# Kernel tuning notes

Hardware: AMD Instinct MI355X
Metric: run time of the kernel (lower is better)

Reference implementation:

```python
import jax, jax.numpy as jnp
import numpy as np

N, E, F, H, L, G = 100000, 1600000, 32, 128, 4, 64


def gru_cell(m, h, w_ih, b_ih, w_hh, b_hh):
    # torch.nn.GRUCell math; gate order: r, z, n
    gi = m @ w_ih.T + b_ih          # [N, 3H]
    gh = h @ w_hh.T + b_hh          # [N, 3H]
    i_r, i_z, i_n = jnp.split(gi, 3, axis=-1)
    h_r, h_z, h_n = jnp.split(gh, 3, axis=-1)
    r = jax.nn.sigmoid(i_r + h_r)
    z = jax.nn.sigmoid(i_z + h_z)
    n = jnp.tanh(i_n + r * h_n)
    return (1.0 - z) * n + z * h


def setup_inputs() -> dict:
    key = jax.random.key(0)
    ks = jax.random.split(key, 12)
    s = 0.05
    return {
        "x": jax.random.normal(ks[0], (N, F), jnp.float32),
        "edge_index": jax.random.randint(ks[1], (2, E), 0, N, jnp.int64),
        "batch": jnp.sort(jax.random.randint(ks[2], (N,), 0, G, jnp.int64)),
        "num_graphs": G,
        "W0": jax.random.normal(ks[3], (H, F), jnp.float32) * s,
        "conv_w": jax.random.normal(ks[4], (L, H, H), jnp.float32) * s,
        "w_ih": jax.random.normal(ks[5], (3 * H, H), jnp.float32) * s,
        "b_ih": jax.random.normal(ks[6], (3 * H,), jnp.float32) * s,
        "w_hh": jax.random.normal(ks[7], (3 * H, H), jnp.float32) * s,
        "b_hh": jax.random.normal(ks[8], (3 * H,), jnp.float32) * s,
        "lin1_w": jax.random.normal(ks[9], (1, H), jnp.float32) * s,
        "lin1_b": jax.random.normal(ks[10], (1,), jnp.float32) * s,
    }


def reference(x, edge_index, batch, num_graphs, W0, conv_w, w_ih, b_ih, w_hh, b_hh, lin1_w, lin1_b):
    n_nodes = x.shape[0]
    # lin0 (no bias) + sigmoid embedding
    x_embed = jax.nn.sigmoid(x @ W0.T)                     # [N, H]

    src, dst = edge_index[0], edge_index[1]
    h = x_embed
    # GatedGraphConv: per layer, transform -> scatter-add over edges -> GRU update
    for l in range(conv_w.shape[0]):
        m = h @ conv_w[l]                                   # [N, H]
        agg = jax.ops.segment_sum(m[src], dst, num_segments=n_nodes)  # [N, H]
        h = gru_cell(agg, h, w_ih, b_ih, w_hh, b_hh)

    h = jax.nn.relu(h)
    out = h @ lin1_w.T + lin1_b                             # [N, 1]
    uncorrected = out

    # per-graph mean subtraction (scatter_mean + gather), same math as the loop
    sums = jax.ops.segment_sum(out, batch, num_segments=num_graphs)   # [G, 1]
    counts = jax.ops.segment_sum(jnp.ones((n_nodes, 1), out.dtype), batch, num_segments=num_graphs)
    mean_all = sums / jnp.maximum(counts, 1.0)
    corrected = out - mean_all[batch]

    return corrected.squeeze(1), x_embed, uncorrected.squeeze(1)
```

## Files before the change

### kernel.cpp

```cpp
#include <hip/hip_runtime.h>
#include <hip/hip_bf16.h>

#define HDIM 128
#define FDIM 32
#define GGR  64
#define SCAN_CHUNK 2048
#define FILL_CHUNK 1024
#define FILL_WIN 16

typedef __attribute__((ext_vector_type(8))) short bf16x8;
typedef __attribute__((ext_vector_type(4))) float f32x4;

__device__ __forceinline__ float fsig(float x) {
  return __builtin_amdgcn_rcpf(1.f + __expf(-x));
}
__device__ __forceinline__ float ftanh(float x) {
  return 1.f - 2.f * __builtin_amdgcn_rcpf(1.f + __expf(2.f * x));
}

__device__ __forceinline__ bf16x8 pack_bf16x8(float4 a, float4 b) {
  union { bf16x8 v; __hip_bfloat162 h[4]; } u;
  u.h[0] = __float22bfloat162_rn(make_float2(a.x, a.y));
  u.h[1] = __float22bfloat162_rn(make_float2(a.z, a.w));
  u.h[2] = __float22bfloat162_rn(make_float2(b.x, b.y));
  u.h[3] = __float22bfloat162_rn(make_float2(b.z, b.w));
  return u.v;
}

__device__ __forceinline__ int ablk(int kb, int m) {
  return (kb << 6) + (m & 56) + ((m ^ kb) & 7);
}

__device__ __forceinline__ void stage64(const unsigned short* __restrict__ g,
                                        short* __restrict__ s, int n0, int N, int t) {
#pragma unroll
  for (int r = 0; r < 2; ++r) {
    int idx = r * 512 + t;
    int m = idx >> 4, c8 = idx & 15;
    int gn = n0 + m;
    uint4 v = make_uint4(0u, 0u, 0u, 0u);
    if (gn < N) v = *(const uint4*)(g + (size_t)gn * HDIM + c8 * 8);
    *(uint4*)(s + ablk(c8, m) * 8) = v;
  }
}


__global__ __launch_bounds__(256) void k_embed_hist(const float* __restrict__ x,
                                                    const unsigned short* __restrict__ W0b,
                                                    unsigned short* __restrict__ hb,
                                                    float* __restrict__ xemb,
                                                    const unsigned short* __restrict__ convT0,
                                                    unsigned short* __restrict__ m_out,
                                                    int N,
                                                    const int* __restrict__ dst,
                                                    int* __restrict__ deg,
                                                    unsigned short* __restrict__ rank,
                                                    long long E, int histBlocks, int q8) {
  __shared__ short sE[16 * 64 * 8];
  if ((int)blockIdx.x < histBlocks) {
    long long e = (long long)blockIdx.x * 256 + threadIdx.x;
    if (e < E) {
      int old = atomicAdd(&deg[dst[e]], 1);
      rank[e] = (unsigned short)old;
    }
    return;
  }
  int p = blockIdx.x - histBlocks;
  int T = (p & 7) * q8 + (p >> 3);
  int n0 = T * 64;
  if (n0 >= N) return;
  int t = threadIdx.x;
  int w = t >> 6, l = t & 63;
  int lm = l & 15, lq = l >> 4;
  int j0 = w * 32;
  bf16x8 b0 = *(const bf16x8*)(W0b + (size_t)(j0 + lm) * FDIM + lq * 8);
  bf16x8 b1 = *(const bf16x8*)(W0b + (size_t)(j0 + 16 + lm) * FDIM + lq * 8);
  f32x4 acc0[4], acc1[4];
#pragma unroll
  for (int i = 0; i < 4; ++i) { acc0[i] = (f32x4){0.f,0.f,0.f,0.f}; acc1[i] = (f32x4){0.f,0.f,0.f,0.f}; }
#pragma unroll
  for (int tt = 0; tt < 4; ++tt) {
    int rg = n0 + tt * 16 + lm;
    bf16x8 a = (bf16x8){0,0,0,0,0,0,0,0};
    if (rg < N) {
      const float4* xr = (const float4*)x + (size_t)rg * 8 + lq * 2;
      a = pack_bf16x8(xr[0], xr[1]);
    }
    acc0[tt] = __builtin_amdgcn_mfma_f32_16x16x32_bf16(a, b0, acc0[tt], 0, 0, 0);
    acc1[tt] = __builtin_amdgcn_mfma_f32_16x16x32_bf16(a, b1, acc1[tt], 0, 0, 0);
  }
#pragma unroll
  for (int g = 0; g < 2; ++g) {
    int j = j0 + g * 16 + lm;
#pragma unroll
    for (int tt = 0; tt < 4; ++tt)
#pragma unroll
      for (int r = 0; r < 4; ++r) {
        int m = tt * 16 + lq * 4 + r;
        int node = n0 + m;
        float v = g ? acc1[tt][r] : acc0[tt][r];
        float e = fsig(v);
        __hip_bfloat16 eb = __float2bfloat16(e);
        ((__hip_bfloat16*)sE)[ablk(j >> 3, m) * 8 + (j & 7)] = eb;
        if (node < N) {
          size_t off = (size_t)node * HDIM + j;
          xemb[off] = e;
          ((__hip_bfloat16*)hb)[off] = eb;
        }
      }
  }
  __syncthreads();
#pragma unroll
  for (int g = 0; g < 2; ++g) {
    int jg = j0 + g * 16;
    f32x4 macc[4];
#pragma unroll
    for (int i = 0; i < 4; ++i) macc[i] = (f32x4){0.f,0.f,0.f,0.f};
#pragma unroll
    for (int ks = 0; ks < 4; ++ks) {
      bf16x8 b = *(const bf16x8*)(convT0 + (size_t)(jg + lm) * HDIM + ks * 32 + lq * 8);
      int kb = ks * 4 + lq;
#pragma unroll
      for (int tt = 0; tt < 4; ++tt) {
        bf16x8 a = *(const bf16x8*)(sE + ablk(kb, tt * 16 + lm) * 8);
        macc[tt] = __builtin_amdgcn_mfma_f32_16x16x32_bf16(a, b, macc[tt], 0, 0, 0);
      }
    }
    int j = jg + lm;
#pragma unroll
    for (int tt = 0; tt < 4; ++tt)
#pragma unroll
      for (int r = 0; r < 4; ++r) {
        int node = n0 + tt * 16 + lq * 4 + r;
        if (node < N)
          ((__hip_bfloat16*)m_out)[(size_t)node * HDIM + j] = __float2bfloat16(macc[tt][r]);
      }
  }
}

__global__ __launch_bounds__(256) void k_prep_w(const float* __restrict__ w_ih,
                                                const float* __restrict__ w_hh,
                                                const float* __restrict__ conv_w,
                                                const float* __restrict__ W0,
                                                unsigned short* __restrict__ wIb,
                                                unsigned short* __restrict__ wHb,
                                                unsigned short* __restrict__ convTb,
                                                unsigned short* __restrict__ W0b,
                                                int L) {
  int i = blockIdx.x * 256 + threadIdx.x;
  if (i < HDIM * FDIM) ((__hip_bfloat16*)W0b)[i] = __float2bfloat16(W0[i]);
  if (i < 384 * HDIM) {
    ((__hip_bfloat16*)wIb)[i] = __float2bfloat16(w_ih[i]);
    ((__hip_bfloat16*)wHb)[i] = __float2bfloat16(w_hh[i]);
  }
  int total = L * HDIM * HDIM;
  if (i < total) {
    int l = i >> 14, rem = i & 16383, j = rem >> 7, k = rem & 127;
    ((__hip_bfloat16*)convTb)[i] = __float2bfloat16(conv_w[(l << 14) + (k << 7) + j]);
  }
}

__global__ __launch_bounds__(256) void k_block_sum(const int* __restrict__ deg,
                                                   int* __restrict__ bsum, int N) {
  int base = blockIdx.x * SCAN_CHUNK + threadIdx.x * 8;
  int s = 0;
#pragma unroll
  for (int u = 0; u < 8; ++u) { int i = base + u; if (i < N) s += deg[i]; }
#pragma unroll
  for (int o = 32; o; o >>= 1) s += __shfl_down(s, o, 64);
  __shared__ int wsum[4];
  if ((threadIdx.x & 63) == 0) wsum[threadIdx.x >> 6] = s;
  __syncthreads();
  if (threadIdx.x == 0) bsum[blockIdx.x] = wsum[0] + wsum[1] + wsum[2] + wsum[3];
}

__global__ void k_scan_bsums(int* __restrict__ bsum, int nb) {
  if (blockIdx.x == 0 && threadIdx.x == 0) {
    int run = 0;
    for (int i = 0; i < nb; ++i) { int v = bsum[i]; bsum[i] = run; run += v; }
  }
}

__global__ __launch_bounds__(256) void k_scan_chunks(const int* __restrict__ deg,
                                                     const int* __restrict__ bsum,
                                                     int* __restrict__ rowstart,
                                                     int N, int Etot) {
  __shared__ int ts[256];
  int base = blockIdx.x * SCAN_CHUNK + threadIdx.x * 8;
  int loc[8]; int s = 0;
#pragma unroll
  for (int u = 0; u < 8; ++u) {
    int i = base + u; loc[u] = s;
    s += (i < N) ? deg[i] : 0;
  }
  ts[threadIdx.x] = s;
  __syncthreads();
  for (int o = 1; o < 256; o <<= 1) {
    int v = (threadIdx.x >= o) ? ts[threadIdx.x - o] : 0;
    __syncthreads();
    ts[threadIdx.x] += v;
    __syncthreads();
  }
  int texcl = (threadIdx.x ? ts[threadIdx.x - 1] : 0) + bsum[blockIdx.x];
#pragma unroll
  for (int u = 0; u < 8; ++u) {
    int i = base + u;
    if (i < N) rowstart[i] = texcl + loc[u];
  }
  if (blockIdx.x == 0 && threadIdx.x == 0) rowstart[N] = Etot;
}

__global__ __launch_bounds__(256) void k_csr_fill_win(const int* __restrict__ src,
                                                      const int* __restrict__ dst,
                                                      const unsigned short* __restrict__ rank,
                                                      const int* __restrict__ rowstart,
                                                      int* __restrict__ csr,
                                                      long long E, int N) {
  __shared__ int sd[FILL_CHUNK];
  __shared__ int ss[FILL_CHUNK];
  __shared__ unsigned short sr[FILL_CHUNK];
  long long base = (long long)blockIdx.x * FILL_CHUNK;
  int cnt = (int)((E - base < FILL_CHUNK) ? (E - base) : FILL_CHUNK);
  for (int i = threadIdx.x; i < cnt; i += 256) {
    sd[i] = dst[base + i];
    ss[i] = src[base + i];
    sr[i] = rank[base + i];
  }
  __syncthreads();
  int nw = (N + FILL_WIN - 1) / FILL_WIN;
#pragma unroll 1
  for (int w = 0; w < FILL_WIN; ++w) {
    int lo = w * nw, hi = lo + nw;
    for (int i = threadIdx.x; i < cnt; i += 256) {
      int d = sd[i];
      if (d >= lo && d < hi)
        csr[rowstart[d] + sr[i]] = ss[i];
    }
    __syncthreads();
  }
}

__global__ __launch_bounds__(256) void k_gather(const int* __restrict__ csr,
                                                const int* __restrict__ rowstart,
                                                const unsigned short* __restrict__ m,
                                                unsigned short* __restrict__ agg, int N, int q8) {
  int p = blockIdx.x;
  int G = (p & 7) * q8 * 16 + (p >> 3);
  int wv = threadIdx.x >> 6, l = threadIdx.x & 63;
  int n = G * 4 + wv;
  if (n >= N) return;
  int eq = l >> 3;
  int jb = l & 7;
  int beg = rowstart[n], end = rowstart[n + 1];
  float acc[16];
#pragma unroll
  for (int i = 0; i < 16; ++i) acc[i] = 0.f;
  for (int e0 = beg; e0 < end; e0 += 8) {
    int e = e0 + eq;
    uint4 v0 = make_uint4(0u, 0u, 0u, 0u);
    uint4 v1 = make_uint4(0u, 0u, 0u, 0u);
    if (e < end) {
      int s = csr[e];
      const uint4* row = (const uint4*)(m + (size_t)s * HDIM + jb * 16);
      v0 = row[0];
      v1 = row[1];
    }
    acc[0]  += __uint_as_float(v0.x << 16);
    acc[1]  += __uint_as_float(v0.x & 0xffff0000u);
    acc[2]  += __uint_as_float(v0.y << 16);
    acc[3]  += __uint_as_float(v0.y & 0xffff0000u);
    acc[4]  += __uint_as_float(v0.z << 16);
    acc[5]  += __uint_as_float(v0.z & 0xffff0000u);
    acc[6]  += __uint_as_float(v0.w << 16);
    acc[7]  += __uint_as_float(v0.w & 0xffff0000u);
    acc[8]  += __uint_as_float(v1.x << 16);
    acc[9]  += __uint_as_float(v1.x & 0xffff0000u);
    acc[10] += __uint_as_float(v1.y << 16);
    acc[11] += __uint_as_float(v1.y & 0xffff0000u);
    acc[12] += __uint_as_float(v1.z << 16);
    acc[13] += __uint_as_float(v1.z & 0xffff0000u);
    acc[14] += __uint_as_float(v1.w << 16);
    acc[15] += __uint_as_float(v1.w & 0xffff0000u);
  }
#pragma unroll
  for (int i = 0; i < 16; ++i) {
    acc[i] += __shfl_xor(acc[i], 8, 64);
    acc[i] += __shfl_xor(acc[i], 16, 64);
    acc[i] += __shfl_xor(acc[i], 32, 64);
  }
  if (eq == 0) {
    union { uint4 v[2]; __hip_bfloat162 h[8]; } o;
#pragma unroll
    for (int i = 0; i < 8; ++i)
      o.h[i] = __float22bfloat162_rn(make_float2(acc[2 * i], acc[2 * i + 1]));
    uint4* dstp = (uint4*)(agg + (size_t)n * HDIM + jb * 16);
    dstp[0] = o.v[0];
    dstp[1] = o.v[1];
  }
}

__global__ __launch_bounds__(512, 4) void k_gru_mfma(const unsigned short* __restrict__ aggb,
                                                  const unsigned short* __restrict__ hb,
                                                  const unsigned short* __restrict__ wI,
                                                  const unsigned short* __restrict__ wH,
                                                  const float* __restrict__ b_ih,
                                                  const float* __restrict__ b_hh,
                                                  unsigned short* __restrict__ hnewb,
                                                  const unsigned short* __restrict__ wT,
                                                  unsigned short* __restrict__ m_out,
                                                  int N, int q8) {
  __shared__ short sAg[16 * 64 * 8];
  __shared__ short sH[16 * 64 * 8];
  int p = blockIdx.x;
  int T = (p & 7) * q8 + (p >> 3);
  int n0 = T * 64;
  if (n0 >= N) return;
  int t = threadIdx.x;
  stage64(aggb, sAg, n0, N, t);
  stage64(hb, sH, n0, N, t);
  int w = t >> 6, l = t & 63;
  int j0 = w * 16;
  int lm = l & 15, lq = l >> 4;
  int j = j0 + lm;
  float bir = b_ih[j], biz = b_ih[j + 128], bin = b_ih[j + 256];
  float bhr = b_hh[j], bhz = b_hh[j + 128], bhn = b_hh[j + 256];
  __syncthreads();
  f32x4 aR[4], aZ[4], aNi[4], aNh[4];
#pragma unroll
  for (int i = 0; i < 4; ++i) {
    aR[i] = (f32x4){0.f,0.f,0.f,0.f}; aZ[i] = (f32x4){0.f,0.f,0.f,0.f};
    aNi[i] = (f32x4){0.f,0.f,0.f,0.f}; aNh[i] = (f32x4){0.f,0.f,0.f,0.f};
  }
#pragma unroll
  for (int ks = 0; ks < 4; ++ks) {
    size_t rI = (size_t)(j0 + lm) * HDIM + ks * 32 + lq * 8;
    bf16x8 bIr = *(const bf16x8*)(wI + rI);
    bf16x8 bIz = *(const bf16x8*)(wI + rI + 128 * HDIM);
    bf16x8 bIn = *(const bf16x8*)(wI + rI + 256 * HDIM);
    bf16x8 bHr = *(const bf16x8*)(wH + rI);
    bf16x8 bHz = *(const bf16x8*)(wH + rI + 128 * HDIM);
    bf16x8 bHn = *(const bf16x8*)(wH + rI + 256 * HDIM);
    int kb = ks * 4 + lq;
#pragma unroll
    for (int tt = 0; tt < 4; ++tt) {
      bf16x8 a = *(const bf16x8*)(sAg + ablk(kb, tt * 16 + lm) * 8);
      bf16x8 h = *(const bf16x8*)(sH + ablk(kb, tt * 16 + lm) * 8);
      aR[tt] = __builtin_amdgcn_mfma_f32_16x16x32_bf16(a, bIr, aR[tt], 0, 0, 0);
      aR[tt] = __builtin_amdgcn_mfma_f32_16x16x32_bf16(h, bHr, aR[tt], 0, 0, 0);
      aZ[tt] = __builtin_amdgcn_mfma_f32_16x16x32_bf16(a, bIz, aZ[tt], 0, 0, 0);
      aZ[tt] = __builtin_amdgcn_mfma_f32_16x16x32_bf16(h, bHz, aZ[tt], 0, 0, 0);
      aNi[tt] = __builtin_amdgcn_mfma_f32_16x16x32_bf16(a, bIn, aNi[tt], 0, 0, 0);
      aNh[tt] = __builtin_amdgcn_mfma_f32_16x16x32_bf16(h, bHn, aNh[tt], 0, 0, 0);
    }
  }
  __syncthreads();
#pragma unroll
  for (int tt = 0; tt < 4; ++tt)
#pragma unroll
    for (int r = 0; r < 4; ++r) {
      int m = tt * 16 + lq * 4 + r;
      int node = n0 + m;
      float hp = __bfloat162float(((const __hip_bfloat16*)sH)[ablk(j >> 3, m) * 8 + (j & 7)]);
      float rg = fsig(aR[tt][r] + bir + bhr);
      float zg = fsig(aZ[tt][r] + biz + bhz);
      float nv = aNi[tt][r] + bin + rg * (aNh[tt][r] + bhn);
      float th = ftanh(nv);
      float hn = (1.f - zg) * th + zg * hp;
      __hip_bfloat16 hnb = __float2bfloat16(hn);
      ((__hip_bfloat16*)sAg)[ablk(j >> 3, m) * 8 + (j & 7)] = hnb;
      if (node < N)
        ((__hip_bfloat16*)hnewb)[(size_t)node * HDIM + j] = hnb;
    }
  __syncthreads();
  f32x4 macc[4];
#pragma unroll
  for (int i = 0; i < 4; ++i) macc[i] = (f32x4){0.f,0.f,0.f,0.f};
#pragma unroll
  for (int ks = 0; ks < 4; ++ks) {
    bf16x8 b = *(const bf16x8*)(wT + (size_t)(j0 + lm) * HDIM + ks * 32 + lq * 8);
    int kb = ks * 4 + lq;
#pragma unroll
    for (int tt = 0; tt < 4; ++tt) {
      bf16x8 a = *(const bf16x8*)(sAg + ablk(kb, tt * 16 + lm) * 8);
      macc[tt] = __builtin_amdgcn_mfma_f32_16x16x32_bf16(a, b, macc[tt], 0, 0, 0);
    }
  }
#pragma unroll
  for (int tt = 0; tt < 4; ++tt)
#pragma unroll
    for (int r = 0; r < 4; ++r) {
      int node = n0 + tt * 16 + lq * 4 + r;
      if (node < N)
        ((__hip_bfloat16*)m_out)[(size_t)node * HDIM + j] = __float2bfloat16(macc[tt][r]);
    }
}

__global__ __launch_bounds__(512, 4) void k_gru_last(const unsigned short* __restrict__ aggb,
                                                  const unsigned short* __restrict__ hb,
                                                  const unsigned short* __restrict__ wI,
                                                  const unsigned short* __restrict__ wH,
                                                  const float* __restrict__ b_ih,
                                                  const float* __restrict__ b_hh,
                                                  const float* __restrict__ w1,
                                                  const float* __restrict__ b1,
                                                  float* __restrict__ out_raw,
                                                  float* __restrict__ out_unc,
                                                  int N, int q8) {
  __shared__ short sAg[16 * 64 * 8];
  __shared__ short sH[16 * 64 * 8];
  __shared__ float sOut[64];
  int p = blockIdx.x;
  int T = (p & 7) * q8 + (p >> 3);
  int n0 = T * 64;
  if (n0 >= N) return;
  int t = threadIdx.x;
  stage64(aggb, sAg, n0, N, t);
  stage64(hb, sH, n0, N, t);
  if (t < 64) sOut[t] = 0.f;
  int w = t >> 6, l = t & 63;
  int j0 = w * 16;
  int lm = l & 15, lq = l >> 4;
  int j = j0 + lm;
  float bir = b_ih[j], biz = b_ih[j + 128], bin = b_ih[j + 256];
  float bhr = b_hh[j], bhz = b_hh[j + 128], bhn = b_hh[j + 256];
  float w1j = w1[j];
  __syncthreads();
  f32x4 aR[4], aZ[4], aNi[4], aNh[4];
#pragma unroll
  for (int i = 0; i < 4; ++i) {
    aR[i] = (f32x4){0.f,0.f,0.f,0.f}; aZ[i] = (f32x4){0.f,0.f,0.f,0.f};
    aNi[i] = (f32x4){0.f,0.f,0.f,0.f}; aNh[i] = (f32x4){0.f,0.f,0.f,0.f};
  }
#pragma unroll
  for (int ks = 0; ks < 4; ++ks) {
    size_t rI = (size_t)(j0 + lm) * HDIM + ks * 32 + lq * 8;
    bf16x8 bIr = *(const bf16x8*)(wI + rI);
    bf16x8 bIz = *(const bf16x8*)(wI + rI + 128 * HDIM);
    bf16x8 bIn = *(const bf16x8*)(wI + rI + 256 * HDIM);
    bf16x8 bHr = *(const bf16x8*)(wH + rI);
    bf16x8 bHz = *(const bf16x8*)(wH + rI + 128 * HDIM);
    bf16x8 bHn = *(const bf16x8*)(wH + rI + 256 * HDIM);
    int kb = ks * 4 + lq;
#pragma unroll
    for (int tt = 0; tt < 4; ++tt) {
      bf16x8 a = *(const bf16x8*)(sAg + ablk(kb, tt * 16 + lm) * 8);
      bf16x8 h = *(const bf16x8*)(sH + ablk(kb, tt * 16 + lm) * 8);
      aR[tt] = __builtin_amdgcn_mfma_f32_16x16x32_bf16(a, bIr, aR[tt], 0, 0, 0);
      aR[tt] = __builtin_amdgcn_mfma_f32_16x16x32_bf16(h, bHr, aR[tt], 0, 0, 0);
      aZ[tt] = __builtin_amdgcn_mfma_f32_16x16x32_bf16(a, bIz, aZ[tt], 0, 0, 0);
      aZ[tt] = __builtin_amdgcn_mfma_f32_16x16x32_bf16(h, bHz, aZ[tt], 0, 0, 0);
      aNi[tt] = __builtin_amdgcn_mfma_f32_16x16x32_bf16(a, bIn, aNi[tt], 0, 0, 0);
      aNh[tt] = __builtin_amdgcn_mfma_f32_16x16x32_bf16(h, bHn, aNh[tt], 0, 0, 0);
    }
  }
  __syncthreads();
#pragma unroll
  for (int tt = 0; tt < 4; ++tt)
#pragma unroll
    for (int r = 0; r < 4; ++r) {
      int m = tt * 16 + lq * 4 + r;
      int node = n0 + m;
      float hp = __bfloat162float(((const __hip_bfloat16*)sH)[ablk(j >> 3, m) * 8 + (j & 7)]);
      float rg = fsig(aR[tt][r] + bir + bhr);
      float zg = fsig(aZ[tt][r] + biz + bhz);
      float nv = aNi[tt][r] + bin + rg * (aNh[tt][r] + bhn);
      float th = ftanh(nv);
      float hn = (1.f - zg) * th + zg * hp;
      float prt = (node < N) ? fmaxf(hn, 0.f) * w1j : 0.f;
      prt += __shfl_xor(prt, 1, 64);
      prt += __shfl_xor(prt, 2, 64);
      prt += __shfl_xor(prt, 4, 64);
      prt += __shfl_xor(prt, 8, 64);
      if (lm == 0) atomicAdd(&sOut[m], prt);
    }
  __syncthreads();
  if (t < 64) {
    int node = n0 + t;
    if (node < N) {
      float o = sOut[t] + b1[0];
      out_raw[node] = o;
      out_unc[node] = o;
    }
  }
}

__global__ __launch_bounds__(256) void k_graph_reduce(const float* __restrict__ out_raw,
                                                      const int* __restrict__ batch,
                                                      float* __restrict__ gsum,
                                                      float* __restrict__ gcnt,
                                                      int N) {
  __shared__ float ls[GGR], lc[GGR];
  int t = threadIdx.x;
  if (t < GGR) { ls[t] = 0.f; lc[t] = 0.f; }
  __syncthreads();
  for (int n = blockIdx.x * 256 + t; n < N; n += gridDim.x * 256) {
    int g = batch[n];
    atomicAdd(&ls[g], out_raw[n]);
    atomicAdd(&lc[g], 1.f);
  }
  __syncthreads();
  if (t < GGR) {
    unsafeAtomicAdd(&gsum[t], ls[t]);
    unsafeAtomicAdd(&gcnt[t], lc[t]);
  }
}

__global__ __launch_bounds__(256) void k_correct(const float* __restrict__ out_raw,
                                                 const int* __restrict__ batch,
                                                 const float* __restrict__ gsum,
                                                 const float* __restrict__ gcnt,
                                                 float* __restrict__ corrected, int N) {
  int n = blockIdx.x * 256 + threadIdx.x;
  if (n < N) {
    int g = batch[n];
    corrected[n] = out_raw[n] - gsum[g] / fmaxf(gcnt[g], 1.f);
  }
}

extern "C" void kernel_launch(void* const* d_in, const int* in_sizes, int n_in,
                              void* d_out, int out_size, void* d_ws, size_t ws_size,
                              hipStream_t stream) {
  const float* x      = (const float*)d_in[0];
  const int*   ei     = (const int*)d_in[1];
  const int*   batch  = (const int*)d_in[2];
  const float* W0     = (const float*)d_in[4];
  const float* conv_w = (const float*)d_in[5];
  const float* w_ih   = (const float*)d_in[6];
  const float* b_ih   = (const float*)d_in[7];
  const float* w_hh   = (const float*)d_in[8];
  const float* b_hh   = (const float*)d_in[9];
  const float* lin1_w = (const float*)d_in[10];
  const float* lin1_b = (const float*)d_in[11];

  int N = in_sizes[0] / FDIM;
  long long E = in_sizes[1] / 2;
  int L = in_sizes[5] / (HDIM * HDIM);

  const int* src = ei;
  const int* dstv = ei + E;

  float* out_corrected = (float*)d_out;
  float* out_xemb = out_corrected + N;
  float* out_unc  = out_xemb + (size_t)N * HDIM;

  char* p = (char*)d_ws;
  unsigned short* x0 = (unsigned short*)p; p += (size_t)N * HDIM * 2;
  unsigned short* x1 = (unsigned short*)p; p += (size_t)N * HDIM * 2;
  unsigned short* x2 = (unsigned short*)p; p += (size_t)N * HDIM * 2;
  float* out_raw = (float*)p;        p += (size_t)((N + 3) & ~3) * 4;
  float* gsum = (float*)p;           p += GGR * 4;
  float* gcnt = (float*)p;           p += GGR * 4;
  int* deg = (int*)p;                p += (size_t)((N + 3) & ~3) * 4;
  int* rowstart = (int*)p;           p += (size_t)(N + 4) * 4;
  int nb = (N + SCAN_CHUNK - 1) / SCAN_CHUNK;
  int* bsum = (int*)p;               p += (size_t)((nb + 63) & ~63) * 4;
  int* csr = (int*)p;                p += (size_t)E * 4;
  unsigned short* rankb = (unsigned short*)p;  p += (size_t)((E + 3) & ~3) * 2;
  unsigned short* wIb = (unsigned short*)p;    p += 384 * HDIM * 2;
  unsigned short* wHb = (unsigned short*)p;    p += 384 * HDIM * 2;
  unsigned short* convTb = (unsigned short*)p; p += (size_t)L * HDIM * HDIM * 2;
  unsigned short* W0b = (unsigned short*)p;

  int prep_total = (384 * HDIM > L * HDIM * HDIM) ? 384 * HDIM : L * HDIM * HDIM;
  k_prep_w<<<(prep_total + 255) / 256, 256, 0, stream>>>(w_ih, w_hh, conv_w, W0, wIb, wHb, convTb, W0b, L);

  hipMemsetAsync(deg, 0, (size_t)N * sizeof(int), stream);
  hipMemsetAsync(gsum, 0, 2 * GGR * sizeof(float), stream);

  int nblk = (N + 63) / 64;
  int TP = (nblk + 7) & ~7;
  int q8 = TP / 8;
  int histBlocks = (int)((E + 255) / 256);
  k_embed_hist<<<histBlocks + TP, 256, 0, stream>>>(x, W0b, x0, out_xemb, convTb, x1, N,
                                                    dstv, deg, rankb, E, histBlocks, q8);

  k_block_sum<<<nb, 256, 0, stream>>>(deg, bsum, N);
  k_scan_bsums<<<1, 64, 0, stream>>>(bsum, nb);
  k_scan_chunks<<<nb, 256, 0, stream>>>(deg, bsum, rowstart, N, (int)E);
  k_csr_fill_win<<<(int)((E + FILL_CHUNK - 1) / FILL_CHUNK), 256, 0, stream>>>(
      src, dstv, rankb, rowstart, csr, E, N);

  unsigned short* Hb = x0;
  unsigned short* Mb = x1;
  for (int l = 0; l < L; ++l) {
    k_gather<<<TP * 16, 256, 0, stream>>>(csr, rowstart, Mb, x2, N, q8);
    if (l + 1 < L) {
      const unsigned short* wTn = convTb + (size_t)(l + 1) * HDIM * HDIM;
      k_gru_mfma<<<TP, 512, 0, stream>>>(x2, Hb, wIb, wHb, b_ih, b_hh, Mb, wTn, Hb, N, q8);
      unsigned short* tmp = Hb; Hb = Mb; Mb = tmp;
    } else {
      k_gru_last<<<TP, 512, 0, stream>>>(x2, Hb, wIb, wHb, b_ih, b_hh,
                                         lin1_w, lin1_b, out_raw, out_unc, N, q8);
    }
  }

  k_graph_reduce<<<256, 256, 0, stream>>>(out_raw, batch, gsum, gcnt, N);
  k_correct<<<(N + 255) / 256, 256, 0, stream>>>(out_raw, batch, gsum, gcnt, out_corrected, N);
}
```

Before: 731.7 us.

## Gather raw hidden states then apply conv weight after aggregation

Uses linearity of the sum over edges: gather and sum h directly, then multiply the summed rows by conv_w[l] inside the GRU kernel, instead of computing m = h@W before the gather. This drops the m_out write from the embed and GRU kernels, along with the separate message buffer. The gather now reads h, and the GRU kernel does one extra 64x128x128 MFMA pass plus extra syncs at its start. Rounding changes because the bf16 sum of h is quantized before the matmul.

```diff
diff --git a/kernel.cpp b/kernel.cpp
--- a/kernel.cpp
+++ b/kernel.cpp
@@ -49,14 +49,11 @@
                                                     const unsigned short* __restrict__ W0b,
                                                     unsigned short* __restrict__ hb,
                                                     float* __restrict__ xemb,
-                                                    const unsigned short* __restrict__ convT0,
-                                                    unsigned short* __restrict__ m_out,
                                                     int N,
                                                     const int* __restrict__ dst,
                                                     int* __restrict__ deg,
                                                     unsigned short* __restrict__ rank,
                                                     long long E, int histBlocks, int q8) {
-  __shared__ short sE[16 * 64 * 8];
   if ((int)blockIdx.x < histBlocks) {
     long long e = (long long)blockIdx.x * 256 + threadIdx.x;
     if (e < E) {
@@ -96,44 +93,14 @@
     for (int tt = 0; tt < 4; ++tt)
 #pragma unroll
       for (int r = 0; r < 4; ++r) {
-        int m = tt * 16 + lq * 4 + r;
-        int node = n0 + m;
-        float v = g ? acc1[tt][r] : acc0[tt][r];
-        float e = fsig(v);
-        __hip_bfloat16 eb = __float2bfloat16(e);
-        ((__hip_bfloat16*)sE)[ablk(j >> 3, m) * 8 + (j & 7)] = eb;
+        int node = n0 + tt * 16 + lq * 4 + r;
         if (node < N) {
+          float v = g ? acc1[tt][r] : acc0[tt][r];
+          float e = fsig(v);
           size_t off = (size_t)node * HDIM + j;
           xemb[off] = e;
-          ((__hip_bfloat16*)hb)[off] = eb;
+          ((__hip_bfloat16*)hb)[off] = __float2bfloat16(e);
         }
-      }
-  }
-  __syncthreads();
-#pragma unroll
-  for (int g = 0; g < 2; ++g) {
-    int jg = j0 + g * 16;
-    f32x4 macc[4];
-#pragma unroll
-    for (int i = 0; i < 4; ++i) macc[i] = (f32x4){0.f,0.f,0.f,0.f};
-#pragma unroll
-    for (int ks = 0; ks < 4; ++ks) {
-      bf16x8 b = *(const bf16x8*)(convT0 + (size_t)(jg + lm) * HDIM + ks * 32 + lq * 8);
-      int kb = ks * 4 + lq;
-#pragma unroll
-      for (int tt = 0; tt < 4; ++tt) {
-        bf16x8 a = *(const bf16x8*)(sE + ablk(kb, tt * 16 + lm) * 8);
-        macc[tt] = __builtin_amdgcn_mfma_f32_16x16x32_bf16(a, b, macc[tt], 0, 0, 0);
-      }
-    }
-    int j = jg + lm;
-#pragma unroll
-    for (int tt = 0; tt < 4; ++tt)
-#pragma unroll
-      for (int r = 0; r < 4; ++r) {
-        int node = n0 + tt * 16 + lq * 4 + r;
-        if (node < N)
-          ((__hip_bfloat16*)m_out)[(size_t)node * HDIM + j] = __float2bfloat16(macc[tt][r]);
       }
   }
 }
@@ -299,15 +266,14 @@
   }
 }
 
-__global__ __launch_bounds__(512, 4) void k_gru_mfma(const unsigned short* __restrict__ aggb,
+__global__ __launch_bounds__(512, 4) void k_gru_mfma(const unsigned short* __restrict__ hsum,
                                                   const unsigned short* __restrict__ hb,
+                                                  const unsigned short* __restrict__ wT,
                                                   const unsigned short* __restrict__ wI,
                                                   const unsigned short* __restrict__ wH,
                                                   const float* __restrict__ b_ih,
                                                   const float* __restrict__ b_hh,
                                                   unsigned short* __restrict__ hnewb,
-                                                  const unsigned short* __restrict__ wT,
-                                                  unsigned short* __restrict__ m_out,
                                                   int N, int q8) {
   __shared__ short sAg[16 * 64 * 8];
   __shared__ short sH[16 * 64 * 8];
@@ -316,7 +282,7 @@
   int n0 = T * 64;
   if (n0 >= N) return;
   int t = threadIdx.x;
-  stage64(aggb, sAg, n0, N, t);
+  stage64(hsum, sAg, n0, N, t);
   stage64(hb, sH, n0, N, t);
   int w = t >> 6, l = t & 63;
   int j0 = w * 16;
@@ -324,6 +290,30 @@
   int j = j0 + lm;
   float bir = b_ih[j], biz = b_ih[j + 128], bin = b_ih[j + 256];
   float bhr = b_hh[j], bhz = b_hh[j + 128], bhn = b_hh[j + 256];
+  __syncthreads();
+  {
+    f32x4 macc[4];
+#pragma unroll
+    for (int i = 0; i < 4; ++i) macc[i] = (f32x4){0.f,0.f,0.f,0.f};
+#pragma unroll
+    for (int ks = 0; ks < 4; ++ks) {
+      bf16x8 b = *(const bf16x8*)(wT + (size_t)(j0 + lm) * HDIM + ks * 32 + lq * 8);
+      int kb = ks * 4 + lq;
+#pragma unroll
+      for (int tt = 0; tt < 4; ++tt) {
+        bf16x8 a = *(const bf16x8*)(sAg + ablk(kb, tt * 16 + lm) * 8);
+        macc[tt] = __builtin_amdgcn_mfma_f32_16x16x32_bf16(a, b, macc[tt], 0, 0, 0);
+      }
+    }
+    __syncthreads();
+#pragma unroll
+    for (int tt = 0; tt < 4; ++tt)
+#pragma unroll
+      for (int r = 0; r < 4; ++r) {
+        int m = tt * 16 + lq * 4 + r;
+        ((__hip_bfloat16*)sAg)[ablk(j >> 3, m) * 8 + (j & 7)] = __float2bfloat16(macc[tt][r]);
+      }
+  }
   __syncthreads();
   f32x4 aR[4], aZ[4], aNi[4], aNh[4];
 #pragma unroll
@@ -353,7 +343,6 @@
       aNh[tt] = __builtin_amdgcn_mfma_f32_16x16x32_bf16(h, bHn, aNh[tt], 0, 0, 0);
     }
   }
-  __syncthreads();
 #pragma unroll
   for (int tt = 0; tt < 4; ++tt)
 #pragma unroll
@@ -366,37 +355,14 @@
       float nv = aNi[tt][r] + bin + rg * (aNh[tt][r] + bhn);
       float th = ftanh(nv);
       float hn = (1.f - zg) * th + zg * hp;
-      __hip_bfloat16 hnb = __float2bfloat16(hn);
-      ((__hip_bfloat16*)sAg)[ablk(j >> 3, m) * 8 + (j & 7)] = hnb;
       if (node < N)
-        ((__hip_bfloat16*)hnewb)[(size_t)node * HDIM + j] = hnb;
-    }
-  __syncthreads();
-  f32x4 macc[4];
-#pragma unroll
-  for (int i = 0; i < 4; ++i) macc[i] = (f32x4){0.f,0.f,0.f,0.f};
-#pragma unroll
-  for (int ks = 0; ks < 4; ++ks) {
-    bf16x8 b = *(const bf16x8*)(wT + (size_t)(j0 + lm) * HDIM + ks * 32 + lq * 8);
-    int kb = ks * 4 + lq;
-#pragma unroll
-    for (int tt = 0; tt < 4; ++tt) {
-      bf16x8 a = *(const bf16x8*)(sAg + ablk(kb, tt * 16 + lm) * 8);
-      macc[tt] = __builtin_amdgcn_mfma_f32_16x16x32_bf16(a, b, macc[tt], 0, 0, 0);
-    }
-  }
-#pragma unroll
-  for (int tt = 0; tt < 4; ++tt)
-#pragma unroll
-    for (int r = 0; r < 4; ++r) {
-      int node = n0 + tt * 16 + lq * 4 + r;
-      if (node < N)
-        ((__hip_bfloat16*)m_out)[(size_t)node * HDIM + j] = __float2bfloat16(macc[tt][r]);
-    }
-}
-
-__global__ __launch_bounds__(512, 4) void k_gru_last(const unsigned short* __restrict__ aggb,
+        ((__hip_bfloat16*)hnewb)[(size_t)node * HDIM + j] = __float2bfloat16(hn);
+    }
+}
+
+__global__ __launch_bounds__(512, 4) void k_gru_last(const unsigned short* __restrict__ hsum,
                                                   const unsigned short* __restrict__ hb,
+                                                  const unsigned short* __restrict__ wT,
                                                   const unsigned short* __restrict__ wI,
                                                   const unsigned short* __restrict__ wH,
                                                   const float* __restrict__ b_ih,
@@ -414,7 +380,7 @@
   int n0 = T * 64;
   if (n0 >= N) return;
   int t = threadIdx.x;
-  stage64(aggb, sAg, n0, N, t);
+  stage64(hsum, sAg, n0, N, t);
   stage64(hb, sH, n0, N, t);
   if (t < 64) sOut[t] = 0.f;
   int w = t >> 6, l = t & 63;
@@ -424,6 +390,30 @@
   float bir = b_ih[j], biz = b_ih[j + 128], bin = b_ih[j + 256];
   float bhr = b_hh[j], bhz = b_hh[j + 128], bhn = b_hh[j + 256];
   float w1j = w1[j];
+  __syncthreads();
+  {
+    f32x4 macc[4];
+#pragma unroll
+    for (int i = 0; i < 4; ++i) macc[i] = (f32x4){0.f,0.f,0.f,0.f};
+#pragma unroll
+    for (int ks = 0; ks < 4; ++ks) {
+      bf16x8 b = *(const bf16x8*)(wT + (size_t)(j0 + lm) * HDIM + ks * 32 + lq * 8);
+      int kb = ks * 4 + lq;
+#pragma unroll
+      for (int tt = 0; tt < 4; ++tt) {
+        bf16x8 a = *(const bf16x8*)(sAg + ablk(kb, tt * 16 + lm) * 8);
+        macc[tt] = __builtin_amdgcn_mfma_f32_16x16x32_bf16(a, b, macc[tt], 0, 0, 0);
+      }
+    }
+    __syncthreads();
+#pragma unroll
+    for (int tt = 0; tt < 4; ++tt)
+#pragma unroll
+      for (int r = 0; r < 4; ++r) {
+        int m = tt * 16 + lq * 4 + r;
+        ((__hip_bfloat16*)sAg)[ablk(j >> 3, m) * 8 + (j & 7)] = __float2bfloat16(macc[tt][r]);
+      }
+  }
   __syncthreads();
   f32x4 aR[4], aZ[4], aNi[4], aNh[4];
 #pragma unroll
@@ -571,7 +561,7 @@
   int TP = (nblk + 7) & ~7;
   int q8 = TP / 8;
   int histBlocks = (int)((E + 255) / 256);
-  k_embed_hist<<<histBlocks + TP, 256, 0, stream>>>(x, W0b, x0, out_xemb, convTb, x1, N,
+  k_embed_hist<<<histBlocks + TP, 256, 0, stream>>>(x, W0b, x0, out_xemb, N,
                                                     dstv, deg, rankb, E, histBlocks, q8);
 
   k_block_sum<<<nb, 256, 0, stream>>>(deg, bsum, N);
@@ -581,15 +571,15 @@
       src, dstv, rankb, rowstart, csr, E, N);
 
   unsigned short* Hb = x0;
-  unsigned short* Mb = x1;
+  unsigned short* Fb = x1;
   for (int l = 0; l < L; ++l) {
-    k_gather<<<TP * 16, 256, 0, stream>>>(csr, rowstart, Mb, x2, N, q8);
+    k_gather<<<TP * 16, 256, 0, stream>>>(csr, rowstart, Hb, x2, N, q8);
+    const unsigned short* wTl = convTb + (size_t)l * HDIM * HDIM;
     if (l + 1 < L) {
-      const unsigned short* wTn = convTb + (size_t)(l + 1) * HDIM * HDIM;
-      k_gru_mfma<<<TP, 512, 0, stream>>>(x2, Hb, wIb, wHb, b_ih, b_hh, Mb, wTn, Hb, N, q8);
-      unsigned short* tmp = Hb; Hb = Mb; Mb = tmp;
+      k_gru_mfma<<<TP, 512, 0, stream>>>(x2, Hb, wTl, wIb, wHb, b_ih, b_hh, Fb, N, q8);
+      unsigned short* tmp = Hb; Hb = Fb; Fb = tmp;
     } else {
-      k_gru_last<<<TP, 512, 0, stream>>>(x2, Hb, wIb, wHb, b_ih, b_hh,
+      k_gru_last<<<TP, 512, 0, stream>>>(x2, Hb, wTl, wIb, wHb, b_ih, b_hh,
                                          lin1_w, lin1_b, out_raw, out_unc, N, q8);
     }
   }
```

New measurement: 715.5 us. 2.2% less time.
